# Kernel tuning notes

Hardware: AMD Instinct MI355X
Metric: run time of the kernel (lower is better)

The kernel has to match this reference:

```python
import jax, jax.numpy as jnp
import numpy as np

B, L, D = 32, 128, 128


def setup_inputs() -> dict:
    key = jax.random.key(0)
    ks = jax.random.split(key, 10)
    s = 1.0 / np.sqrt(D)  # torch nn.Linear default init bound
    inp = {
        "input_real": jax.random.normal(ks[0], (B, L, D), jnp.float32),
        "input_imag": jax.random.normal(ks[1], (B, L, D), jnp.float32),
        "Wr1": jax.random.uniform(ks[2], (D, D), jnp.float32, -s, s),
        "br1": jax.random.uniform(ks[3], (D,), jnp.float32, -s, s),
        "Wi1": jax.random.uniform(ks[4], (D, D), jnp.float32, -s, s),
        "bi1": jax.random.uniform(ks[5], (D,), jnp.float32, -s, s),
        "Wr2": jax.random.uniform(ks[6], (D, D), jnp.float32, -s, s),
        "br2": jax.random.uniform(ks[7], (D,), jnp.float32, -s, s),
        "Wi2": jax.random.uniform(ks[8], (D, D), jnp.float32, -s, s),
        "bi2": jax.random.uniform(ks[9], (D,), jnp.float32, -s, s),
    }
    return inp


def reference(input_real, input_imag, Wr1, br1, Wi1, bi1, Wr2, br2, Wi2, bi2):
    # torch Linear: y = x @ W.T + b
    r1 = input_real @ Wr1.T + br1            # (B, L, D)
    i1 = input_imag @ Wi1.T + bi1
    diag_real1 = r1 * r1 - i1 * i1           # Re((r1+i*i1)^2)
    diag_imag1 = 2.0 * r1 * i1               # Im((r1+i*i1)^2)

    r2 = input_real @ Wr2.T + br2
    i2 = input_imag @ Wi2.T + bi2
    diag_real2 = r2 * r2 - i2 * i2
    diag_imag2 = 2.0 * r2 * i2

    # attention over sequence positions L
    att_real = jax.nn.softmax(jnp.sum(diag_real1 * diag_real2, axis=-1), axis=-1)  # (B, L)
    att_imag = jax.nn.softmax(jnp.sum(diag_imag1 * diag_imag2, axis=-1), axis=-1)  # (B, L)

    # Weighted sum over L of per-token complex outer products, without
    # materializing the (B, L, D, D) intermediates the torch code builds:
    # Matrix_real[l] = r2 r2^T - i2 i2^T ; Matrix_imag[l] = i2 r2^T + r2 i2^T
    Mr = (jnp.einsum('bl,bld,ble->bde', att_real, r2, r2)
          - jnp.einsum('bl,bld,ble->bde', att_real, i2, i2))   # (B, D, D)
    Mi = (jnp.einsum('bl,bld,ble->bde', att_imag, i2, r2)
          + jnp.einsum('bl,bld,ble->bde', att_imag, r2, i2))   # (B, D, D)
    return (Mr, Mi)
```

## Files before the change

### kernel.cpp

```cpp
#include <hip/hip_runtime.h>
#include <hip/hip_bf16.h>
#include <math.h>

#define NB 32
#define NL 128
#define ND 128

typedef __attribute__((ext_vector_type(8))) short bf16x8;
typedef __attribute__((ext_vector_type(4))) float f32x4;

union F4 { float4 v; float f[4]; };

__device__ inline ushort f2bf(float f) {
    __hip_bfloat16 h = __float2bfloat16(f);
    union { __hip_bfloat16 h; ushort u; } c; c.h = h; return c.u;
}
__device__ inline float bf2f(ushort u) {
    union { unsigned int i; float f; } c; c.i = ((unsigned int)u) << 16; return c.f;
}
__device__ inline short2 bsplit(float f) {
    ushort hu = f2bf(f);
    short2 r;
    r.x = (short)hu;
    r.y = (short)f2bf(f - bf2f(hu));
    return r;
}

__global__ __launch_bounds__(256) void k_proj(
    const float* __restrict__ xr, const float* __restrict__ xi,
    const float* __restrict__ Wr1, const float* __restrict__ br1,
    const float* __restrict__ Wi1, const float* __restrict__ bi1,
    const float* __restrict__ Wr2, const float* __restrict__ br2,
    const float* __restrict__ Wi2, const float* __restrict__ bi2,
    float* __restrict__ partR, float* __restrict__ partI,
    ushort* __restrict__ r2tb, ushort* __restrict__ i2tb)
{
    __shared__ char XhB[8192];
    __shared__ char XlB[8192];
    __shared__ char WhB[16384];
    __shared__ char WlB[16384];

    const int t    = threadIdx.x;
    const int tile = blockIdx.x >> 1;
    const int half = blockIdx.x & 1;
    const int d0   = half * 64;
    const int w    = t >> 6;
    const int lane = t & 63;

    const int slot = t & 15;
    const int tr   = t >> 4;

    {
        const float* xs[2] = {xr, xi};
#pragma unroll
        for (int arr = 0; arr < 2; ++arr) {
            const float* Xb = xs[arr] + (size_t)(tile * 16 + tr) * ND + slot * 8;
            F4 f0, f1; f0.v = *(const float4*)&Xb[0]; f1.v = *(const float4*)&Xb[4];
            bf16x8 h, l;
#pragma unroll
            for (int e = 0; e < 4; ++e) {
                short2 s = bsplit(f0.f[e]); h[e] = s.x; l[e] = s.y;
            }
#pragma unroll
            for (int e = 0; e < 4; ++e) {
                short2 s = bsplit(f1.f[e]); h[4 + e] = s.x; l[4 + e] = s.y;
            }
            int byte = arr * 4096 + tr * 256 + ((slot * 16) ^ ((tr & 7) << 4));
            *(bf16x8*)(XhB + byte) = h;
            *(bf16x8*)(XlB + byte) = l;
        }
    }

    F4 wpa[4], wpb[4];
#define LOADW(WP)                                                             \
    _Pragma("unroll")                                                         \
    for (int j = 0; j < 4; ++j) {                                             \
        const float* p = WP + (size_t)(d0 + j * 16 + tr) * ND + slot * 8;     \
        wpa[j].v = *(const float4*)&p[0];                                     \
        wpb[j].v = *(const float4*)&p[4];                                     \
    }
    LOADW(Wr1)

    __syncthreads();

    const int arow  = lane & 15;
    const int koffb = (lane >> 4) * 16;
    bf16x8 axh[8], axl[8];
#pragma unroll
    for (int arr = 0; arr < 2; ++arr)
#pragma unroll
        for (int ks = 0; ks < 4; ++ks) {
            int byte = arr * 4096 + arow * 256 +
                       (((ks * 64) + koffb) ^ ((arow & 7) << 4));
            axh[arr * 4 + ks] = *(const bf16x8*)(XhB + byte);
            axl[arr * 4 + ks] = *(const bf16x8*)(XlB + byte);
        }

    f32x4 acc[4];
#pragma unroll
    for (int m = 0; m < 4; ++m) acc[m] = (f32x4){0.f, 0.f, 0.f, 0.f};

    const int brow = w * 16 + (lane & 15);

#pragma unroll
    for (int mat = 0; mat < 4; ++mat) {
        __syncthreads();
#pragma unroll
        for (int j = 0; j < 4; ++j) {
            bf16x8 h, l;
#pragma unroll
            for (int e = 0; e < 4; ++e) {
                short2 s = bsplit(wpa[j].f[e]); h[e] = s.x; l[e] = s.y;
            }
#pragma unroll
            for (int e = 0; e < 4; ++e) {
                short2 s = bsplit(wpb[j].f[e]); h[4 + e] = s.x; l[4 + e] = s.y;
            }
            int row  = j * 16 + tr;
            int byte = row * 256 + ((slot * 16) ^ ((row & 7) << 4));
            *(bf16x8*)(WhB + byte) = h;
            *(bf16x8*)(WlB + byte) = l;
        }
        if (mat == 0)      { LOADW(Wi1) }
        else if (mat == 1) { LOADW(Wr2) }
        else if (mat == 2) { LOADW(Wi2) }
        __syncthreads();

        const int arr = mat & 1;
#pragma unroll
        for (int ks = 0; ks < 4; ++ks) {
            bf16x8 ah = axh[arr * 4 + ks];
            bf16x8 al = axl[arr * 4 + ks];
            int bbyte = brow * 256 + (((ks * 64) + koffb) ^ ((brow & 7) << 4));
            bf16x8 bh = *(const bf16x8*)(WhB + bbyte);
            bf16x8 bl = *(const bf16x8*)(WlB + bbyte);
            acc[mat] = __builtin_amdgcn_mfma_f32_16x16x32_bf16(ah, bh, acc[mat], 0, 0, 0);
            acc[mat] = __builtin_amdgcn_mfma_f32_16x16x32_bf16(ah, bl, acc[mat], 0, 0, 0);
            acc[mat] = __builtin_amdgcn_mfma_f32_16x16x32_bf16(al, bh, acc[mat], 0, 0, 0);
        }
    }
#undef LOADW

    const int d = d0 + w * 16 + (lane & 15);
    const float b0v = br1[d], b1v = bi1[d], b2v = br2[d], b3v = bi2[d];

    float y0[4], y1[4], y2[4], y3[4];
#pragma unroll
    for (int r = 0; r < 4; ++r) {
        y0[r] = acc[0][r] + b0v;
        y1[r] = acc[1][r] + b1v;
        y2[r] = acc[2][r] + b2v;
        y3[r] = acc[3][r] + b3v;
    }

    float pR[4], pI[4];
#pragma unroll
    for (int r = 0; r < 4; ++r) {
        float A  = y0[r] * y0[r] - y1[r] * y1[r];
        float Bv = y2[r] * y2[r] - y3[r] * y3[r];
        pR[r] = A * Bv;
        pI[r] = 4.f * y0[r] * y1[r] * y2[r] * y3[r];
    }
#pragma unroll
    for (int off = 1; off < 16; off <<= 1) {
#pragma unroll
        for (int r = 0; r < 4; ++r) {
            pR[r] += __shfl_xor(pR[r], off);
            pI[r] += __shfl_xor(pI[r], off);
        }
    }
    if ((lane & 15) == 0) {
        const int s    = half * 4 + w;
        const int base = tile * 16 + (lane >> 4) * 4;
        float4 vR = {pR[0], pR[1], pR[2], pR[3]};
        float4 vI = {pI[0], pI[1], pI[2], pI[3]};
        *(float4*)&partR[(size_t)s * 4096 + base] = vR;
        *(float4*)&partI[(size_t)s * 4096 + base] = vI;
    }

    {
        const int b  = tile >> 3;
        const int lb = (tile & 7) * 16 + (lane >> 4) * 4;
        ushort4 p2 = {f2bf(y2[0]), f2bf(y2[1]), f2bf(y2[2]), f2bf(y2[3])};
        ushort4 p3 = {f2bf(y3[0]), f2bf(y3[1]), f2bf(y3[2]), f2bf(y3[3])};
        *(ushort4*)&r2tb[(size_t)b * ND * NL + (size_t)d * NL + lb] = p2;
        *(ushort4*)&i2tb[(size_t)b * ND * NL + (size_t)d * NL + lb] = p3;
    }
}

__global__ __launch_bounds__(256) void k_gram(
    const ushort* __restrict__ r2tb, const ushort* __restrict__ i2tb,
    const float* __restrict__ partR, const float* __restrict__ partI,
    float* __restrict__ out)
{
    __shared__ char As[2][16384];
    __shared__ char Bs[2][8192];
    __shared__ float lgs[128];
    __shared__ float swf[128];

    const int t    = threadIdx.x;
    const int bid  = blockIdx.x;
    const int b    = bid >> 4;
    const int term = (bid >> 3) & 1;
    const int dq   = (bid >> 2) & 1;
    const int eo   = bid & 3;

    const float* part = term ? partI : partR;
    if (t < 128) {
        float s = 0.f;
#pragma unroll
        for (int k = 0; k < 8; ++k) s += part[(size_t)k * 4096 + b * NL + t];
        lgs[t] = s;
    }
    __syncthreads();
    float m = -3.4e38f;
    for (int i = 0; i < NL; ++i) m = fmaxf(m, lgs[i]);
    float ssum = 0.f;
    for (int i = 0; i < NL; ++i) ssum += expf(lgs[i] - m);
    if (t < 128) swf[t] = sqrtf(expf(lgs[t] - m) / ssum);
    __syncthreads();

    const int slot = t & 15;
    float swv[8];
#pragma unroll
    for (int e = 0; e < 8; ++e) swv[e] = swf[slot * 8 + e];

    const ushort* srcs[2] = {r2tb, i2tb};
#pragma unroll
    for (int j = 0; j < 8; ++j) {
        int g   = t + 256 * j;
        int arr = g >> 10;
        int row = (g >> 4) & 63;
        const ushort* src = srcs[arr] + (size_t)b * ND * NL;
        bf16x8 v = *(const bf16x8*)&src[(size_t)(dq * 64 + row) * NL + slot * 8];
        bf16x8 x;
#pragma unroll
        for (int e = 0; e < 8; ++e)
            x[e] = (short)f2bf(bf2f((ushort)v[e]) * swv[e]);
        *(bf16x8*)(As[arr] + row * 256 + ((slot * 16) ^ ((row & 7) << 4))) = x;
    }
#pragma unroll
    for (int j = 0; j < 4; ++j) {
        int g   = t + 256 * j;
        int arr = g >> 9;
        int row = (g >> 4) & 31;
        const ushort* src = srcs[arr] + (size_t)b * ND * NL;
        bf16x8 v = *(const bf16x8*)&src[(size_t)(eo * 32 + row) * NL + slot * 8];
        bf16x8 x;
#pragma unroll
        for (int e = 0; e < 8; ++e)
            x[e] = (short)f2bf(bf2f((ushort)v[e]) * swv[e]);
        *(bf16x8*)(Bs[arr] + row * 256 + ((slot * 16) ^ ((row & 7) << 4))) = x;
    }
    __syncthreads();

    const int w    = t >> 6;
    const int lane = t & 63;
    const int arow = w * 16 + (lane & 15);
    const int koff = (lane >> 4) * 16;

    f32x4 accP[2], accN[2];
#pragma unroll
    for (int nt = 0; nt < 2; ++nt) {
        accP[nt] = (f32x4){0.f, 0.f, 0.f, 0.f};
        accN[nt] = (f32x4){0.f, 0.f, 0.f, 0.f};
    }

#pragma unroll
    for (int ks = 0; ks < 4; ++ks) {
        const int abyte = arow * 256 + (((ks * 64) + koff) ^ ((arow & 7) << 4));
        bf16x8 a0 = *(const bf16x8*)(As[0] + abyte);
        bf16x8 a1 = *(const bf16x8*)(As[1] + abyte);
        bf16x8 aP = term ? a1 : a0;
        bf16x8 aN = term ? a0 : a1;
#pragma unroll
        for (int nt = 0; nt < 2; ++nt) {
            const int brw   = nt * 16 + (lane & 15);
            const int bbyte = brw * 256 + (((ks * 64) + koff) ^ ((brw & 7) << 4));
            bf16x8 b0 = *(const bf16x8*)(Bs[0] + bbyte);
            bf16x8 b1 = *(const bf16x8*)(Bs[1] + bbyte);
            accP[nt] = __builtin_amdgcn_mfma_f32_16x16x32_bf16(aP, b0, accP[nt], 0, 0, 0);
            accN[nt] = __builtin_amdgcn_mfma_f32_16x16x32_bf16(aN, b1, accN[nt], 0, 0, 0);
        }
    }

    const float sgn = term ? 1.f : -1.f;
    float* dst = out + (size_t)term * NB * ND * ND + (size_t)b * ND * ND;
    const int drow = dq * 64 + w * 16 + (lane >> 4) * 4;
#pragma unroll
    for (int nt = 0; nt < 2; ++nt) {
        const int ecol = eo * 32 + nt * 16 + (lane & 15);
#pragma unroll
        for (int r = 0; r < 4; ++r)
            dst[(size_t)(drow + r) * ND + ecol] = accP[nt][r] + sgn * accN[nt][r];
    }
}

extern "C" void kernel_launch(void* const* d_in, const int* in_sizes, int n_in,
                              void* d_out, int out_size, void* d_ws, size_t ws_size,
                              hipStream_t stream)
{
    const float* xr  = (const float*)d_in[0];
    const float* xi  = (const float*)d_in[1];
    const float* Wr1 = (const float*)d_in[2];
    const float* br1 = (const float*)d_in[3];
    const float* Wi1 = (const float*)d_in[4];
    const float* bi1 = (const float*)d_in[5];
    const float* Wr2 = (const float*)d_in[6];
    const float* br2 = (const float*)d_in[7];
    const float* Wi2 = (const float*)d_in[8];
    const float* bi2 = (const float*)d_in[9];

    float* ws    = (float*)d_ws;
    float* partR = ws;
    float* partI = ws + 8 * 4096;
    ushort* r2tb = (ushort*)(ws + 16 * 4096);
    ushort* i2tb = r2tb + (size_t)NB * ND * NL;

    hipLaunchKernelGGL(k_proj, dim3(512), dim3(256), 0, stream,
                       xr, xi, Wr1, br1, Wi1, bi1, Wr2, br2, Wi2, bi2,
                       partR, partI, r2tb, i2tb);
    hipLaunchKernelGGL(k_gram, dim3(512), dim3(256), 0, stream,
                       r2tb, i2tb, partR, partI, (float*)d_out);
}
```

Measured before the change: 28.34 us.

## Fuse projection, softmax and gram into one per-batch kernel with presplit weights

Replaces the projection and gram kernels with a small weight pre-split kernel plus one fused kernel per batch. Each 512-thread block computes all four projections for its batch, keeps r2/i2 in LDS as bf16, computes the softmax in-block, and runs the weighted gram product directly, with no global intermediates. This removes the workspace round trip, the second heavy launch and the redundant softmax work. The cost is only 32 blocks on a large GPU, very high register pressure (many accumulators), and the weights being read from global memory by every block.

```diff
diff --git a/kernel.cpp b/kernel.cpp
--- a/kernel.cpp
+++ b/kernel.cpp
@@ -9,7 +9,8 @@
 typedef __attribute__((ext_vector_type(8))) short bf16x8;
 typedef __attribute__((ext_vector_type(4))) float f32x4;
 
-union F4 { float4 v; float f[4]; };
+union F4  { float4 v; float f[4]; };
+union BF8 { bf16x8 v; ushort u[8]; };
 
 __device__ inline ushort f2bf(float f) {
     __hip_bfloat16 h = __float2bfloat16(f);
@@ -26,273 +27,224 @@
     return r;
 }
 
-__global__ __launch_bounds__(256) void k_proj(
+__global__ __launch_bounds__(256) void k_wsplit(
+    const float* __restrict__ Wr1, const float* __restrict__ Wi1,
+    const float* __restrict__ Wr2, const float* __restrict__ Wi2,
+    ushort* __restrict__ whg, ushort* __restrict__ wlg)
+{
+    const int mat   = blockIdx.x >> 4;
+    const int chunk = blockIdx.x & 15;
+    const float* W = (mat == 0) ? Wr1 : (mat == 1) ? Wi1 : (mat == 2) ? Wr2 : Wi2;
+    const int idx = chunk * 1024 + threadIdx.x * 4;
+    F4 v; v.v = *(const float4*)&W[idx];
+    short2 s0 = bsplit(v.f[0]), s1 = bsplit(v.f[1]);
+    short2 s2 = bsplit(v.f[2]), s3 = bsplit(v.f[3]);
+    ushort4 h = {(ushort)s0.x, (ushort)s1.x, (ushort)s2.x, (ushort)s3.x};
+    ushort4 l = {(ushort)s0.y, (ushort)s1.y, (ushort)s2.y, (ushort)s3.y};
+    *(ushort4*)&whg[mat * 16384 + idx] = h;
+    *(ushort4*)&wlg[mat * 16384 + idx] = l;
+}
+
+__global__ __launch_bounds__(512, 2) void k_fused(
     const float* __restrict__ xr, const float* __restrict__ xi,
-    const float* __restrict__ Wr1, const float* __restrict__ br1,
-    const float* __restrict__ Wi1, const float* __restrict__ bi1,
-    const float* __restrict__ Wr2, const float* __restrict__ br2,
-    const float* __restrict__ Wi2, const float* __restrict__ bi2,
-    float* __restrict__ partR, float* __restrict__ partI,
-    ushort* __restrict__ r2tb, ushort* __restrict__ i2tb)
+    const ushort* __restrict__ whg, const ushort* __restrict__ wlg,
+    const float* __restrict__ br1, const float* __restrict__ bi1,
+    const float* __restrict__ br2, const float* __restrict__ bi2,
+    float* __restrict__ out)
 {
-    __shared__ char XhB[8192];
-    __shared__ char XlB[8192];
-    __shared__ char WhB[16384];
-    __shared__ char WlB[16384];
-
-    const int t    = threadIdx.x;
-    const int tile = blockIdx.x >> 1;
-    const int half = blockIdx.x & 1;
-    const int d0   = half * 64;
-    const int w    = t >> 6;
-    const int lane = t & 63;
-
-    const int slot = t & 15;
-    const int tr   = t >> 4;
-
+    extern __shared__ char L[];
+    char*  Gm   = L;
+    float* lgs  = (float*)(L + 65536);
+    float* wfl  = (float*)(L + 66560);
+    float* wred = (float*)(L + 67584);
+
+    const int t     = threadIdx.x;
+    const int b     = blockIdx.x;
+    const int w     = t >> 6;
+    const int lane  = t & 63;
+    const int l15   = lane & 15;
+    const int koff8 = (lane >> 4) * 8;
+    const int koffb = koff8 * 2;
+    const int arow  = w * 16 + l15;
+    const int lb    = w * 16 + (lane >> 4) * 4;
+
+    bf16x8 axh[2][4], axl[2][4];
     {
         const float* xs[2] = {xr, xi};
 #pragma unroll
-        for (int arr = 0; arr < 2; ++arr) {
-            const float* Xb = xs[arr] + (size_t)(tile * 16 + tr) * ND + slot * 8;
-            F4 f0, f1; f0.v = *(const float4*)&Xb[0]; f1.v = *(const float4*)&Xb[4];
-            bf16x8 h, l;
-#pragma unroll
-            for (int e = 0; e < 4; ++e) {
-                short2 s = bsplit(f0.f[e]); h[e] = s.x; l[e] = s.y;
-            }
-#pragma unroll
-            for (int e = 0; e < 4; ++e) {
-                short2 s = bsplit(f1.f[e]); h[4 + e] = s.x; l[4 + e] = s.y;
-            }
-            int byte = arr * 4096 + tr * 256 + ((slot * 16) ^ ((tr & 7) << 4));
-            *(bf16x8*)(XhB + byte) = h;
-            *(bf16x8*)(XlB + byte) = l;
-        }
-    }
-
-    F4 wpa[4], wpb[4];
-#define LOADW(WP)                                                             \
-    _Pragma("unroll")                                                         \
-    for (int j = 0; j < 4; ++j) {                                             \
-        const float* p = WP + (size_t)(d0 + j * 16 + tr) * ND + slot * 8;     \
-        wpa[j].v = *(const float4*)&p[0];                                     \
-        wpb[j].v = *(const float4*)&p[4];                                     \
-    }
-    LOADW(Wr1)
-
-    __syncthreads();
-
-    const int arow  = lane & 15;
-    const int koffb = (lane >> 4) * 16;
-    bf16x8 axh[8], axl[8];
-#pragma unroll
-    for (int arr = 0; arr < 2; ++arr)
-#pragma unroll
-        for (int ks = 0; ks < 4; ++ks) {
-            int byte = arr * 4096 + arow * 256 +
-                       (((ks * 64) + koffb) ^ ((arow & 7) << 4));
-            axh[arr * 4 + ks] = *(const bf16x8*)(XhB + byte);
-            axl[arr * 4 + ks] = *(const bf16x8*)(XlB + byte);
-        }
-
-    f32x4 acc[4];
-#pragma unroll
-    for (int m = 0; m < 4; ++m) acc[m] = (f32x4){0.f, 0.f, 0.f, 0.f};
-
-    const int brow = w * 16 + (lane & 15);
+        for (int arr = 0; arr < 2; ++arr)
+#pragma unroll
+            for (int ks = 0; ks < 4; ++ks) {
+                const float* p = xs[arr] + (size_t)(b * NL + arow) * ND + ks * 32 + koff8;
+                F4 f0, f1;
+                f0.v = *(const float4*)&p[0];
+                f1.v = *(const float4*)&p[4];
+                bf16x8 h, l;
+#pragma unroll
+                for (int e = 0; e < 4; ++e) {
+                    short2 s = bsplit(f0.f[e]); h[e] = s.x; l[e] = s.y;
+                }
+#pragma unroll
+                for (int e = 0; e < 4; ++e) {
+                    short2 s = bsplit(f1.f[e]); h[4 + e] = s.x; l[4 + e] = s.y;
+                }
+                axh[arr][ks] = h;
+                axl[arr][ks] = l;
+            }
+    }
+
+    f32x4 acc[4][8];
+#pragma unroll
+    for (int m = 0; m < 4; ++m)
+#pragma unroll
+        for (int nt = 0; nt < 8; ++nt) acc[m][nt] = (f32x4){0.f, 0.f, 0.f, 0.f};
 
 #pragma unroll
     for (int mat = 0; mat < 4; ++mat) {
-        __syncthreads();
-#pragma unroll
-        for (int j = 0; j < 4; ++j) {
-            bf16x8 h, l;
-#pragma unroll
-            for (int e = 0; e < 4; ++e) {
-                short2 s = bsplit(wpa[j].f[e]); h[e] = s.x; l[e] = s.y;
-            }
-#pragma unroll
-            for (int e = 0; e < 4; ++e) {
-                short2 s = bsplit(wpb[j].f[e]); h[4 + e] = s.x; l[4 + e] = s.y;
-            }
-            int row  = j * 16 + tr;
-            int byte = row * 256 + ((slot * 16) ^ ((row & 7) << 4));
-            *(bf16x8*)(WhB + byte) = h;
-            *(bf16x8*)(WlB + byte) = l;
-        }
-        if (mat == 0)      { LOADW(Wi1) }
-        else if (mat == 1) { LOADW(Wr2) }
-        else if (mat == 2) { LOADW(Wi2) }
-        __syncthreads();
-
         const int arr = mat & 1;
 #pragma unroll
-        for (int ks = 0; ks < 4; ++ks) {
-            bf16x8 ah = axh[arr * 4 + ks];
-            bf16x8 al = axl[arr * 4 + ks];
-            int bbyte = brow * 256 + (((ks * 64) + koffb) ^ ((brow & 7) << 4));
-            bf16x8 bh = *(const bf16x8*)(WhB + bbyte);
-            bf16x8 bl = *(const bf16x8*)(WlB + bbyte);
-            acc[mat] = __builtin_amdgcn_mfma_f32_16x16x32_bf16(ah, bh, acc[mat], 0, 0, 0);
-            acc[mat] = __builtin_amdgcn_mfma_f32_16x16x32_bf16(ah, bl, acc[mat], 0, 0, 0);
-            acc[mat] = __builtin_amdgcn_mfma_f32_16x16x32_bf16(al, bh, acc[mat], 0, 0, 0);
-        }
-    }
-#undef LOADW
-
-    const int d = d0 + w * 16 + (lane & 15);
-    const float b0v = br1[d], b1v = bi1[d], b2v = br2[d], b3v = bi2[d];
-
-    float y0[4], y1[4], y2[4], y3[4];
-#pragma unroll
-    for (int r = 0; r < 4; ++r) {
-        y0[r] = acc[0][r] + b0v;
-        y1[r] = acc[1][r] + b1v;
-        y2[r] = acc[2][r] + b2v;
-        y3[r] = acc[3][r] + b3v;
-    }
-
-    float pR[4], pI[4];
-#pragma unroll
-    for (int r = 0; r < 4; ++r) {
-        float A  = y0[r] * y0[r] - y1[r] * y1[r];
-        float Bv = y2[r] * y2[r] - y3[r] * y3[r];
-        pR[r] = A * Bv;
-        pI[r] = 4.f * y0[r] * y1[r] * y2[r] * y3[r];
-    }
-#pragma unroll
-    for (int off = 1; off < 16; off <<= 1) {
+        for (int nt = 0; nt < 8; ++nt) {
+            const ushort* wp = whg + mat * 16384 + (nt * 16 + l15) * 128 + koff8;
+            const ushort* lp = wlg + mat * 16384 + (nt * 16 + l15) * 128 + koff8;
+#pragma unroll
+            for (int ks = 0; ks < 4; ++ks) {
+                bf16x8 bh = *(const bf16x8*)&wp[ks * 32];
+                bf16x8 bl = *(const bf16x8*)&lp[ks * 32];
+                acc[mat][nt] = __builtin_amdgcn_mfma_f32_16x16x32_bf16(axh[arr][ks], bh, acc[mat][nt], 0, 0, 0);
+                acc[mat][nt] = __builtin_amdgcn_mfma_f32_16x16x32_bf16(axh[arr][ks], bl, acc[mat][nt], 0, 0, 0);
+                acc[mat][nt] = __builtin_amdgcn_mfma_f32_16x16x32_bf16(axl[arr][ks], bh, acc[mat][nt], 0, 0, 0);
+            }
+        }
+    }
+
+    float pR[4] = {0.f, 0.f, 0.f, 0.f};
+    float pI[4] = {0.f, 0.f, 0.f, 0.f};
+#pragma unroll
+    for (int nt = 0; nt < 8; ++nt) {
+        const int d = nt * 16 + l15;
+        const float b0 = br1[d], b1 = bi1[d], b2 = br2[d], b3 = bi2[d];
+        ushort g2[4], g3[4];
+#pragma unroll
+        for (int r = 0; r < 4; ++r) {
+            float y0 = acc[0][nt][r] + b0;
+            float y1 = acc[1][nt][r] + b1;
+            float y2 = acc[2][nt][r] + b2;
+            float y3 = acc[3][nt][r] + b3;
+            pR[r] += (y0 * y0 - y1 * y1) * (y2 * y2 - y3 * y3);
+            pI[r] += 4.f * y0 * y1 * y2 * y3;
+            g2[r] = f2bf(y2);
+            g3[r] = f2bf(y3);
+        }
+        const int byte0 = d * 256 + ((lb * 2) ^ ((d & 7) << 4));
+        *(unsigned int*)(Gm + byte0)             = (unsigned int)g2[0] | ((unsigned int)g2[1] << 16);
+        *(unsigned int*)(Gm + byte0 + 4)         = (unsigned int)g2[2] | ((unsigned int)g2[3] << 16);
+        *(unsigned int*)(Gm + 32768 + byte0)     = (unsigned int)g3[0] | ((unsigned int)g3[1] << 16);
+        *(unsigned int*)(Gm + 32768 + byte0 + 4) = (unsigned int)g3[2] | ((unsigned int)g3[3] << 16);
+    }
+
+#pragma unroll
+    for (int off = 1; off < 16; off <<= 1)
 #pragma unroll
         for (int r = 0; r < 4; ++r) {
             pR[r] += __shfl_xor(pR[r], off);
             pI[r] += __shfl_xor(pI[r], off);
         }
-    }
-    if ((lane & 15) == 0) {
-        const int s    = half * 4 + w;
-        const int base = tile * 16 + (lane >> 4) * 4;
-        float4 vR = {pR[0], pR[1], pR[2], pR[3]};
-        float4 vI = {pI[0], pI[1], pI[2], pI[3]};
-        *(float4*)&partR[(size_t)s * 4096 + base] = vR;
-        *(float4*)&partI[(size_t)s * 4096 + base] = vI;
-    }
-
-    {
-        const int b  = tile >> 3;
-        const int lb = (tile & 7) * 16 + (lane >> 4) * 4;
-        ushort4 p2 = {f2bf(y2[0]), f2bf(y2[1]), f2bf(y2[2]), f2bf(y2[3])};
-        ushort4 p3 = {f2bf(y3[0]), f2bf(y3[1]), f2bf(y3[2]), f2bf(y3[3])};
-        *(ushort4*)&r2tb[(size_t)b * ND * NL + (size_t)d * NL + lb] = p2;
-        *(ushort4*)&i2tb[(size_t)b * ND * NL + (size_t)d * NL + lb] = p3;
-    }
-}
-
-__global__ __launch_bounds__(256) void k_gram(
-    const ushort* __restrict__ r2tb, const ushort* __restrict__ i2tb,
-    const float* __restrict__ partR, const float* __restrict__ partI,
-    float* __restrict__ out)
-{
-    __shared__ char As[2][16384];
-    __shared__ char Bs[2][8192];
-    __shared__ float lgs[128];
-    __shared__ float swf[128];
-
-    const int t    = threadIdx.x;
-    const int bid  = blockIdx.x;
-    const int b    = bid >> 4;
-    const int term = (bid >> 3) & 1;
-    const int dq   = (bid >> 2) & 1;
-    const int eo   = bid & 3;
-
-    const float* part = term ? partI : partR;
-    if (t < 128) {
-        float s = 0.f;
-#pragma unroll
-        for (int k = 0; k < 8; ++k) s += part[(size_t)k * 4096 + b * NL + t];
-        lgs[t] = s;
-    }
-    __syncthreads();
-    float m = -3.4e38f;
-    for (int i = 0; i < NL; ++i) m = fmaxf(m, lgs[i]);
-    float ssum = 0.f;
-    for (int i = 0; i < NL; ++i) ssum += expf(lgs[i] - m);
-    if (t < 128) swf[t] = sqrtf(expf(lgs[t] - m) / ssum);
-    __syncthreads();
-
-    const int slot = t & 15;
-    float swv[8];
-#pragma unroll
-    for (int e = 0; e < 8; ++e) swv[e] = swf[slot * 8 + e];
-
-    const ushort* srcs[2] = {r2tb, i2tb};
-#pragma unroll
-    for (int j = 0; j < 8; ++j) {
-        int g   = t + 256 * j;
-        int arr = g >> 10;
-        int row = (g >> 4) & 63;
-        const ushort* src = srcs[arr] + (size_t)b * ND * NL;
-        bf16x8 v = *(const bf16x8*)&src[(size_t)(dq * 64 + row) * NL + slot * 8];
-        bf16x8 x;
-#pragma unroll
-        for (int e = 0; e < 8; ++e)
-            x[e] = (short)f2bf(bf2f((ushort)v[e]) * swv[e]);
-        *(bf16x8*)(As[arr] + row * 256 + ((slot * 16) ^ ((row & 7) << 4))) = x;
-    }
-#pragma unroll
-    for (int j = 0; j < 4; ++j) {
-        int g   = t + 256 * j;
-        int arr = g >> 9;
-        int row = (g >> 4) & 31;
-        const ushort* src = srcs[arr] + (size_t)b * ND * NL;
-        bf16x8 v = *(const bf16x8*)&src[(size_t)(eo * 32 + row) * NL + slot * 8];
-        bf16x8 x;
-#pragma unroll
-        for (int e = 0; e < 8; ++e)
-            x[e] = (short)f2bf(bf2f((ushort)v[e]) * swv[e]);
-        *(bf16x8*)(Bs[arr] + row * 256 + ((slot * 16) ^ ((row & 7) << 4))) = x;
-    }
-    __syncthreads();
-
-    const int w    = t >> 6;
-    const int lane = t & 63;
-    const int arow = w * 16 + (lane & 15);
-    const int koff = (lane >> 4) * 16;
-
-    f32x4 accP[2], accN[2];
-#pragma unroll
-    for (int nt = 0; nt < 2; ++nt) {
-        accP[nt] = (f32x4){0.f, 0.f, 0.f, 0.f};
-        accN[nt] = (f32x4){0.f, 0.f, 0.f, 0.f};
-    }
+    if (l15 == 0) {
+#pragma unroll
+        for (int r = 0; r < 4; ++r) {
+            lgs[lb + r]       = pR[r];
+            lgs[128 + lb + r] = pI[r];
+        }
+    }
+    __syncthreads();
+
+    float sv = 0.f, se = 0.f;
+    const int c = t >> 7;
+    if (t < 256) {
+        sv = lgs[c * 128 + (t & 127)];
+        float m = sv;
+#pragma unroll
+        for (int off = 1; off < 64; off <<= 1) m = fmaxf(m, __shfl_xor(m, off));
+        if (lane == 0) wred[t >> 6] = m;
+    }
+    __syncthreads();
+    if (t < 256) {
+        float m = fmaxf(wred[c * 2], wred[c * 2 + 1]);
+        se = expf(sv - m);
+        float s = se;
+#pragma unroll
+        for (int off = 1; off < 64; off <<= 1) s += __shfl_xor(s, off);
+        if (lane == 0) wred[4 + (t >> 6)] = s;
+    }
+    __syncthreads();
+    if (t < 256) {
+        float s = wred[4 + c * 2] + wred[4 + c * 2 + 1];
+        wfl[c * 128 + (t & 127)] = se / s;
+    }
+    __syncthreads();
+
+    const int term = w >> 2;
+    const int mt0  = (w & 3) * 2;
+
+    f32x4 accP[2][8], accN[2][8];
+#pragma unroll
+    for (int m = 0; m < 2; ++m)
+#pragma unroll
+        for (int nt = 0; nt < 8; ++nt) {
+            accP[m][nt] = (f32x4){0.f, 0.f, 0.f, 0.f};
+            accN[m][nt] = (f32x4){0.f, 0.f, 0.f, 0.f};
+        }
 
 #pragma unroll
     for (int ks = 0; ks < 4; ++ks) {
-        const int abyte = arow * 256 + (((ks * 64) + koff) ^ ((arow & 7) << 4));
-        bf16x8 a0 = *(const bf16x8*)(As[0] + abyte);
-        bf16x8 a1 = *(const bf16x8*)(As[1] + abyte);
-        bf16x8 aP = term ? a1 : a0;
-        bf16x8 aN = term ? a0 : a1;
-#pragma unroll
-        for (int nt = 0; nt < 2; ++nt) {
-            const int brw   = nt * 16 + (lane & 15);
-            const int bbyte = brw * 256 + (((ks * 64) + koff) ^ ((brw & 7) << 4));
-            bf16x8 b0 = *(const bf16x8*)(Bs[0] + bbyte);
-            bf16x8 b1 = *(const bf16x8*)(Bs[1] + bbyte);
-            accP[nt] = __builtin_amdgcn_mfma_f32_16x16x32_bf16(aP, b0, accP[nt], 0, 0, 0);
-            accN[nt] = __builtin_amdgcn_mfma_f32_16x16x32_bf16(aN, b1, accN[nt], 0, 0, 0);
+        F4 w0, w1;
+        w0.v = *(const float4*)&wfl[term * 128 + ks * 32 + koff8];
+        w1.v = *(const float4*)&wfl[term * 128 + ks * 32 + koff8 + 4];
+        float wv[8] = {w0.f[0], w0.f[1], w0.f[2], w0.f[3],
+                       w1.f[0], w1.f[1], w1.f[2], w1.f[3]};
+
+        bf16x8 aP[2], aN[2];
+#pragma unroll
+        for (int m = 0; m < 2; ++m) {
+            const int ar = (mt0 + m) * 16 + l15;
+            const int ab = ar * 256 + (((ks * 64) + koffb) ^ ((ar & 7) << 4));
+            BF8 a0; a0.v = *(const bf16x8*)(Gm + ab);
+            BF8 a1; a1.v = *(const bf16x8*)(Gm + 32768 + ab);
+            bf16x8 s0, s1;
+#pragma unroll
+            for (int e = 0; e < 8; ++e) {
+                s0[e] = (short)f2bf(bf2f(a0.u[e]) * wv[e]);
+                s1[e] = (short)f2bf(bf2f(a1.u[e]) * wv[e]);
+            }
+            aP[m] = term ? s1 : s0;
+            aN[m] = term ? s0 : s1;
+        }
+#pragma unroll
+        for (int nt = 0; nt < 8; ++nt) {
+            const int br = nt * 16 + l15;
+            const int bb = br * 256 + (((ks * 64) + koffb) ^ ((br & 7) << 4));
+            bf16x8 b0 = *(const bf16x8*)(Gm + bb);
+            bf16x8 b1 = *(const bf16x8*)(Gm + 32768 + bb);
+#pragma unroll
+            for (int m = 0; m < 2; ++m) {
+                accP[m][nt] = __builtin_amdgcn_mfma_f32_16x16x32_bf16(aP[m], b0, accP[m][nt], 0, 0, 0);
+                accN[m][nt] = __builtin_amdgcn_mfma_f32_16x16x32_bf16(aN[m], b1, accN[m][nt], 0, 0, 0);
+            }
         }
     }
 
     const float sgn = term ? 1.f : -1.f;
     float* dst = out + (size_t)term * NB * ND * ND + (size_t)b * ND * ND;
-    const int drow = dq * 64 + w * 16 + (lane >> 4) * 4;
-#pragma unroll
-    for (int nt = 0; nt < 2; ++nt) {
-        const int ecol = eo * 32 + nt * 16 + (lane & 15);
-#pragma unroll
-        for (int r = 0; r < 4; ++r)
-            dst[(size_t)(drow + r) * ND + ecol] = accP[nt][r] + sgn * accN[nt][r];
+#pragma unroll
+    for (int m = 0; m < 2; ++m) {
+        const int rb = (mt0 + m) * 16 + (lane >> 4) * 4;
+#pragma unroll
+        for (int nt = 0; nt < 8; ++nt) {
+            const int ec = nt * 16 + l15;
+#pragma unroll
+            for (int r = 0; r < 4; ++r)
+                dst[(size_t)(rb + r) * ND + ec] = accP[m][nt][r] + sgn * accN[m][nt][r];
+        }
     }
 }
 
@@ -311,15 +263,15 @@
     const float* Wi2 = (const float*)d_in[8];
     const float* bi2 = (const float*)d_in[9];
 
-    float* ws    = (float*)d_ws;
-    float* partR = ws;
-    float* partI = ws + 8 * 4096;
-    ushort* r2tb = (ushort*)(ws + 16 * 4096);
-    ushort* i2tb = r2tb + (size_t)NB * ND * NL;
-
-    hipLaunchKernelGGL(k_proj, dim3(512), dim3(256), 0, stream,
-                       xr, xi, Wr1, br1, Wi1, bi1, Wr2, br2, Wi2, bi2,
-                       partR, partI, r2tb, i2tb);
-    hipLaunchKernelGGL(k_gram, dim3(512), dim3(256), 0, stream,
-                       r2tb, i2tb, partR, partI, (float*)d_out);
-}
+    ushort* whg = (ushort*)d_ws;
+    ushort* wlg = whg + 4 * 16384;
+
+    (void)hipFuncSetAttribute((const void*)k_fused,
+                              hipFuncAttributeMaxDynamicSharedMemorySize, 67648);
+
+    hipLaunchKernelGGL(k_wsplit, dim3(64), dim3(256), 0, stream,
+                       Wr1, Wi1, Wr2, Wi2, whg, wlg);
+    hipLaunchKernelGGL(k_fused, dim3(NB), dim3(512), 67648, stream,
+                       xr, xi, whg, wlg, br1, bi1, br2, bi2,
+                       (float*)d_out);
+}
```

New measurement: 77.58 us. +173.8%, slower.
